# Performance work log

Measured on AMD Instinct MI355X. Metric: run time of the kernel, lower is better.

The kernel has to match this reference:

```python
import jax, jax.numpy as jnp
import numpy as np

B, D, M, C = 1024, 64, 3, 16384

def setup_inputs() -> dict:
    key = jax.random.key(0)
    ks = jax.random.split(key, 8)
    # unit-norm features (as in contrastive learning) keep exp() in range
    f = jax.random.normal(ks[0], (B, D), jnp.float32)
    f_I = jax.random.normal(ks[1], (B, D), jnp.float32)
    f = f / jnp.linalg.norm(f, axis=1, keepdims=True)
    f_I = f_I / jnp.linalg.norm(f_I, axis=1, keepdims=True)
    cen = jax.random.normal(ks[2], (M, C, D), jnp.float32)
    cen_I = jax.random.normal(ks[3], (M, C, D), jnp.float32)
    cen = cen / jnp.linalg.norm(cen, axis=2, keepdims=True)
    cen_I = cen_I / jnp.linalg.norm(cen_I, axis=2, keepdims=True)
    # concentrations in [0.5, 1.5): positive temperatures
    conc = jax.random.uniform(ks[4], (M, C), jnp.float32) + 0.5
    conc_I = jax.random.uniform(ks[5], (M, C), jnp.float32) + 0.5
    lab = jax.random.randint(ks[6], (M, B), 0, C, jnp.int64 if jax.config.jax_enable_x64 else jnp.int32)
    lab_I = jax.random.randint(ks[7], (M, B), 0, C, jnp.int64 if jax.config.jax_enable_x64 else jnp.int32)
    return {"features": f, "features_I": f_I, "M_kmeans": cen, "M_kmeans_I": cen_I,
            "concentrations": conc, "concentrations_I": conc_I,
            "labels": lab, "labels_I": lab_I, "lb": 1}

def _branch_loss(centroids, feats, conc, labels):
    # centroids: [M,C,D], feats: [B,D], conc: [M,C], labels: [M,B]
    # logits[m,c,b] = (centroids[m,c] . feats[b]) / conc[m,c]
    logits = jnp.einsum('mcd,bd->mcb', centroids, feats) / conc[:, :, None]
    exp_logits = jnp.exp(logits)                       # [M,C,B]
    log_sum = jnp.sum(exp_logits, axis=1)              # [M,B]
    pos = jnp.take_along_axis(exp_logits, labels[:, None, :], axis=1)[:, 0, :]  # [M,B]
    return jnp.sum(jnp.log(pos / log_sum))             # scalar (summed over m and b)

def reference(features, features_I, M_kmeans, M_kmeans_I,
              concentrations, concentrations_I, labels, labels_I, lb):
    m_num = M_kmeans.shape[0]
    batch_size = features.shape[0]
    t = _branch_loss(M_kmeans, features_I, concentrations, labels)
    t_I = _branch_loss(M_kmeans_I, features, concentrations_I, labels_I)
    return (1.0 / batch_size) * lb * (-1.0 / m_num) * 0.5 * (t + t_I)
```

## Files before the change

### kernel.cpp

```cpp
#include <hip/hip_runtime.h>

#define B_   1024
#define D_   64
#define M_   3
#define C_   16384
#define NCH  32
#define CCH  (C_ / NCH)
#define NTL  (CCH / 16)

typedef __attribute__((ext_vector_type(8))) short bf16x8;
typedef __attribute__((ext_vector_type(4))) float f32x4;

__device__ __forceinline__ unsigned bfpack2(float lo, float hi) {
    return __builtin_amdgcn_perm(__float_as_uint(hi), __float_as_uint(lo),
                                 0x07060302u);
}
__device__ __forceinline__ bf16x8 pack8(float4 x, float4 y) {
    union { unsigned u[4]; bf16x8 v; } r;
    r.u[0] = bfpack2(x.x, x.y);
    r.u[1] = bfpack2(x.z, x.w);
    r.u[2] = bfpack2(y.x, y.y);
    r.u[3] = bfpack2(y.z, y.w);
    return r.v;
}
__device__ __forceinline__ float fexp2(float x) {
    float r; asm("v_exp_f32 %0, %1" : "=v"(r) : "v"(x)); return r;
}
__device__ __forceinline__ void gll16(const void* g, void* l) {
    __builtin_amdgcn_global_load_lds(
        (const __attribute__((address_space(1))) void*)g,
        (__attribute__((address_space(3))) void*)l, 16, 0, 0);
}


__global__ __launch_bounds__(256) void prep(
    const float* __restrict__ f, const float* __restrict__ f_I,
    unsigned short* __restrict__ fbf)
{
    const int t    = blockIdx.x * 256 + threadIdx.x;
    const int br   = t >> 13;
    const int r    = t & 8191;
    const int bt   = r >> 7;
    const int h    = (r >> 6) & 1;
    const int lane = r & 63;
    const int b    = bt * 16 + (lane & 15);
    const int d0   = h * 32 + (lane >> 4) * 8;
    const float* src = (br ? f : f_I) + (size_t)b * D_ + d0;
    const float4 x = *reinterpret_cast<const float4*>(src);
    const float4 y = *reinterpret_cast<const float4*>(src + 4);
    *reinterpret_cast<bf16x8*>(fbf + (size_t)t * 8) = pack8(x, y);
}

__global__ __launch_bounds__(256, 3) void lse_mfma(
    const float* __restrict__ cen0, const float* __restrict__ cen1,
    const unsigned short* __restrict__ fbf,
    const float* __restrict__ conc0, const float* __restrict__ conc1,
    float* __restrict__ wsum)
{
    __shared__ float tbuf[2][1024];
    __shared__ float cbuf[CCH];
    __shared__ float lsum[4][64];

    const int bid    = blockIdx.x;
    const int xcd    = bid & 7;
    const int i2     = bid >> 3;
    const int pp     = i2 >> 2;
    const int bblk   = i2 & 3;
    const int combo  = xcd * 24 + pp;
    const int cchunk = combo & 31;
    const int mbr    = combo >> 5;
    const int br = mbr & 1, m = mbr >> 1;

    const float* __restrict__ cen  = br ? cen1  : cen0;
    const float* __restrict__ conc = br ? conc1 : conc0;

    const int tid  = threadIdx.x;
    const int wv   = tid >> 6;
    const int lane = tid & 63;
    const int lrow = lane & 15;
    const int lk   = lane >> 4;
    const int wbase = bblk * 256 + wv * 64;
    const float LOG2E = 1.44269504088896340736f;

    const unsigned short* fbb = fbf + (size_t)br * 8192 * 8;
    bf16x8 af[4][2];
#pragma unroll
    for (int t = 0; t < 4; ++t)
#pragma unroll
        for (int h = 0; h < 2; ++h)
            af[t][h] = *reinterpret_cast<const bf16x8*>(
                fbb + ((size_t)(((wbase >> 4) + t) * 2 + h) * 64 + lane) * 8);

    const int cb = cchunk * CCH;
    const int srow = tid >> 4;
    const int soff = ((tid & 15) << 4) ^ ((srow & 7) << 4);
    const char* csrc = (const char*)(cen + ((size_t)m * C_ + cb) * D_)
                     + srow * 256 + soff;

    gll16(csrc, (char*)tbuf[0] + wv * 1024);
    if (tid < 128)
        gll16((const char*)(conc + (size_t)m * C_ + cb) + tid * 16,
              (char*)cbuf + wv * 1024);
    __syncthreads();

    float s[4][4];
#pragma unroll
    for (int t = 0; t < 4; ++t)
#pragma unroll
        for (int j = 0; j < 4; ++j) s[t][j] = 0.0f;

    const unsigned swz = (unsigned)((lrow & 7) << 4);
    int cur = 0;
    for (int ct = 0; ct < NTL; ++ct) {
        if (ct + 1 < NTL)
            gll16(csrc + (size_t)(ct + 1) * 4096,
                  (char*)tbuf[cur ^ 1] + wv * 1024);

        const char* bp = (const char*)tbuf[cur] + lrow * 256;
        const float4 r00 = *(const float4*)(bp + ((lk * 32      ) ^ swz));
        const float4 r01 = *(const float4*)(bp + ((lk * 32 + 16 ) ^ swz));
        const float4 r10 = *(const float4*)(bp + ((128 + lk * 32     ) ^ swz));
        const float4 r11 = *(const float4*)(bp + ((128 + lk * 32 + 16) ^ swz));
        const float  cc  = cbuf[ct * 16 + lrow];

        const bf16x8 bk0 = pack8(r00, r01);
        const bf16x8 bk1 = pack8(r10, r11);
        const float  ic  = LOG2E * __builtin_amdgcn_rcpf(cc);

        f32x4 a0 = {0.f,0.f,0.f,0.f}, a1 = {0.f,0.f,0.f,0.f};
        f32x4 a2 = {0.f,0.f,0.f,0.f}, a3 = {0.f,0.f,0.f,0.f};
        a0 = __builtin_amdgcn_mfma_f32_16x16x32_bf16(af[0][0], bk0, a0, 0, 0, 0);
        a0 = __builtin_amdgcn_mfma_f32_16x16x32_bf16(af[0][1], bk1, a0, 0, 0, 0);
        a1 = __builtin_amdgcn_mfma_f32_16x16x32_bf16(af[1][0], bk0, a1, 0, 0, 0);
        a1 = __builtin_amdgcn_mfma_f32_16x16x32_bf16(af[1][1], bk1, a1, 0, 0, 0);
        a2 = __builtin_amdgcn_mfma_f32_16x16x32_bf16(af[2][0], bk0, a2, 0, 0, 0);
        a2 = __builtin_amdgcn_mfma_f32_16x16x32_bf16(af[2][1], bk1, a2, 0, 0, 0);
        a3 = __builtin_amdgcn_mfma_f32_16x16x32_bf16(af[3][0], bk0, a3, 0, 0, 0);
        a3 = __builtin_amdgcn_mfma_f32_16x16x32_bf16(af[3][1], bk1, a3, 0, 0, 0);

#pragma unroll
        for (int j = 0; j < 4; ++j) {
            s[0][j] += fexp2(a0[j] * ic);
            s[1][j] += fexp2(a1[j] * ic);
            s[2][j] += fexp2(a2[j] * ic);
            s[3][j] += fexp2(a3[j] * ic);
        }

        __syncthreads();
        cur ^= 1;
    }

#pragma unroll
    for (int t = 0; t < 4; ++t)
#pragma unroll
        for (int j = 0; j < 4; ++j) {
            float v = s[t][j];
            v += __shfl_xor(v, 1);
            v += __shfl_xor(v, 2);
            v += __shfl_xor(v, 4);
            v += __shfl_xor(v, 8);
            s[t][j] = v;
        }
    if (lrow == 0) {
#pragma unroll
        for (int t = 0; t < 4; ++t)
#pragma unroll
            for (int j = 0; j < 4; ++j)
                lsum[wv][t * 16 + lk * 4 + j] = s[t][j];
    }
    __syncthreads();
    atomicAdd(&wsum[(size_t)(br * M_ + m) * B_ + bblk * 256 + tid],
              lsum[tid >> 6][tid & 63]);
}

__global__ __launch_bounds__(256) void finish(
    const float* __restrict__ f,    const float* __restrict__ f_I,
    const float* __restrict__ cen0, const float* __restrict__ cen1,
    const float* __restrict__ conc0,const float* __restrict__ conc1,
    const int*   __restrict__ lab0, const int*   __restrict__ lab1,
    const float* __restrict__ wsum, const int* __restrict__ lb,
    float* __restrict__ out)
{
    const int idx = blockIdx.x * 256 + threadIdx.x;
    const int br  = idx / (M_ * B_);
    const int r   = idx - br * (M_ * B_);
    const int m   = r / B_;
    const int b   = r - m * B_;

    const float* cen  = br ? cen1  : cen0;
    const float* conc = br ? conc1 : conc0;
    const int*   lab  = br ? lab1  : lab0;
    const float* ft   = br ? f     : f_I;

    const int c = lab[r];
    const float* cr   = cen + (size_t)(m * C_ + c) * D_;
    const float* frow = ft + (size_t)b * D_;
    float a0 = 0.f, a1 = 0.f, a2 = 0.f, a3 = 0.f;
#pragma unroll
    for (int d = 0; d < D_; d += 4) {
        a0 = fmaf(cr[d + 0], frow[d + 0], a0);
        a1 = fmaf(cr[d + 1], frow[d + 1], a1);
        a2 = fmaf(cr[d + 2], frow[d + 2], a2);
        a3 = fmaf(cr[d + 3], frow[d + 3], a3);
    }
    const float logit = ((a0 + a1) + (a2 + a3)) / conc[(size_t)m * C_ + c];
    float term = logit - __logf(wsum[idx]);

#pragma unroll
    for (int off = 32; off > 0; off >>= 1)
        term += __shfl_down(term, off);
    if ((threadIdx.x & 63) == 0) {
        const float scale = -0.5f * (float)lb[0] / (float)(B_ * M_);
        atomicAdd(out, scale * term);
    }
}

extern "C" void kernel_launch(void* const* d_in, const int* in_sizes, int n_in,
                              void* d_out, int out_size, void* d_ws, size_t ws_size,
                              hipStream_t stream) {
    const float* f      = (const float*)d_in[0];
    const float* f_I    = (const float*)d_in[1];
    const float* cen    = (const float*)d_in[2];
    const float* cen_I  = (const float*)d_in[3];
    const float* conc   = (const float*)d_in[4];
    const float* conc_I = (const float*)d_in[5];
    const int*   lab    = (const int*)d_in[6];
    const int*   lab_I  = (const int*)d_in[7];
    const int*   lb     = (const int*)d_in[8];

    float* ws   = (float*)d_ws;
    float* wsum = ws;
    unsigned short* fbf = (unsigned short*)(ws + 6144);
    float* out  = (float*)d_out;

    hipMemsetAsync(wsum, 0, 6144 * sizeof(float), stream);
    hipMemsetAsync(out, 0, sizeof(float), stream);

    prep<<<64, 256, 0, stream>>>(f, f_I, fbf);

    lse_mfma<<<768, 256, 0, stream>>>(cen, cen_I, fbf, conc, conc_I, wsum);

    finish<<<(2 * M_ * B_) / 256, 256, 0, stream>>>(
        f, f_I, cen, cen_I, conc, conc_I, lab, lab_I, wsum, lb, out);
}
```

Measured before the change: 125.4 us.

## Stage 64-row centroid tiles per barrier and fold memsets into prep kernel

Each pipeline stage now loads 64 centroid rows (four 16-row subtiles) into a larger double-buffered LDS area, so there are four times fewer barriers per chunk. Concentrations are now read straight from global memory instead of being staged in LDS. The two hipMemsetAsync calls are removed and their zeroing moves into the prep kernel, which cuts launch overhead. The cost is higher LDS use per block (32KB of tile buffers), which may reduce occupancy.

New measurement: 118.3 us. -5.7%, faster.

```diff
diff --git a/kernel.cpp b/kernel.cpp
--- a/kernel.cpp
+++ b/kernel.cpp
@@ -6,7 +6,8 @@
 #define C_   16384
 #define NCH  32
 #define CCH  (C_ / NCH)
-#define NTL  (CCH / 16)
+#define TROWS 64
+#define NTL  (CCH / TROWS)
 
 typedef __attribute__((ext_vector_type(8))) short bf16x8;
 typedef __attribute__((ext_vector_type(4))) float f32x4;
@@ -35,7 +36,8 @@
 
 __global__ __launch_bounds__(256) void prep(
     const float* __restrict__ f, const float* __restrict__ f_I,
-    unsigned short* __restrict__ fbf)
+    unsigned short* __restrict__ fbf, float* __restrict__ wsum,
+    float* __restrict__ out)
 {
     const int t    = blockIdx.x * 256 + threadIdx.x;
     const int br   = t >> 13;
@@ -49,6 +51,8 @@
     const float4 x = *reinterpret_cast<const float4*>(src);
     const float4 y = *reinterpret_cast<const float4*>(src + 4);
     *reinterpret_cast<bf16x8*>(fbf + (size_t)t * 8) = pack8(x, y);
+    if (t < 2 * M_ * B_) wsum[t] = 0.0f;
+    if (t == 16383) out[0] = 0.0f;
 }
 
 __global__ __launch_bounds__(256, 3) void lse_mfma(
@@ -57,8 +61,7 @@
     const float* __restrict__ conc0, const float* __restrict__ conc1,
     float* __restrict__ wsum)
 {
-    __shared__ float tbuf[2][1024];
-    __shared__ float cbuf[CCH];
+    __shared__ float tbuf[2][4096];
     __shared__ float lsum[4][64];
 
     const int bid    = blockIdx.x;
@@ -92,15 +95,18 @@
                 fbb + ((size_t)(((wbase >> 4) + t) * 2 + h) * 64 + lane) * 8);
 
     const int cb = cchunk * CCH;
-    const int srow = tid >> 4;
-    const int soff = ((tid & 15) << 4) ^ ((srow & 7) << 4);
-    const char* csrc = (const char*)(cen + ((size_t)m * C_ + cb) * D_)
-                     + srow * 256 + soff;
-
-    gll16(csrc, (char*)tbuf[0] + wv * 1024);
-    if (tid < 128)
-        gll16((const char*)(conc + (size_t)m * C_ + cb) + tid * 16,
-              (char*)cbuf + wv * 1024);
+    const char* cbase = (const char*)(cen + ((size_t)m * C_ + cb) * D_);
+    int soff[4];
+#pragma unroll
+    for (int s2 = 0; s2 < 4; ++s2) {
+        const int row = s2 * 16 + (tid >> 4);
+        soff[s2] = row * 256 + ((((tid & 15) << 4)) ^ ((row & 7) << 4));
+    }
+    const int dseg = wv * 1024;
+
+#pragma unroll
+    for (int s2 = 0; s2 < 4; ++s2)
+        gll16(cbase + soff[s2], (char*)tbuf[0] + s2 * 4096 + dseg);
     __syncthreads();
 
     float s[4][4];
@@ -110,42 +116,47 @@
         for (int j = 0; j < 4; ++j) s[t][j] = 0.0f;
 
     const unsigned swz = (unsigned)((lrow & 7) << 4);
+    const float* ccp = conc + (size_t)m * C_ + cb + lrow;
     int cur = 0;
     for (int ct = 0; ct < NTL; ++ct) {
-        if (ct + 1 < NTL)
-            gll16(csrc + (size_t)(ct + 1) * 4096,
-                  (char*)tbuf[cur ^ 1] + wv * 1024);
-
-        const char* bp = (const char*)tbuf[cur] + lrow * 256;
-        const float4 r00 = *(const float4*)(bp + ((lk * 32      ) ^ swz));
-        const float4 r01 = *(const float4*)(bp + ((lk * 32 + 16 ) ^ swz));
-        const float4 r10 = *(const float4*)(bp + ((128 + lk * 32     ) ^ swz));
-        const float4 r11 = *(const float4*)(bp + ((128 + lk * 32 + 16) ^ swz));
-        const float  cc  = cbuf[ct * 16 + lrow];
-
-        const bf16x8 bk0 = pack8(r00, r01);
-        const bf16x8 bk1 = pack8(r10, r11);
-        const float  ic  = LOG2E * __builtin_amdgcn_rcpf(cc);
-
-        f32x4 a0 = {0.f,0.f,0.f,0.f}, a1 = {0.f,0.f,0.f,0.f};
-        f32x4 a2 = {0.f,0.f,0.f,0.f}, a3 = {0.f,0.f,0.f,0.f};
-        a0 = __builtin_amdgcn_mfma_f32_16x16x32_bf16(af[0][0], bk0, a0, 0, 0, 0);
-        a0 = __builtin_amdgcn_mfma_f32_16x16x32_bf16(af[0][1], bk1, a0, 0, 0, 0);
-        a1 = __builtin_amdgcn_mfma_f32_16x16x32_bf16(af[1][0], bk0, a1, 0, 0, 0);
-        a1 = __builtin_amdgcn_mfma_f32_16x16x32_bf16(af[1][1], bk1, a1, 0, 0, 0);
-        a2 = __builtin_amdgcn_mfma_f32_16x16x32_bf16(af[2][0], bk0, a2, 0, 0, 0);
-        a2 = __builtin_amdgcn_mfma_f32_16x16x32_bf16(af[2][1], bk1, a2, 0, 0, 0);
-        a3 = __builtin_amdgcn_mfma_f32_16x16x32_bf16(af[3][0], bk0, a3, 0, 0, 0);
-        a3 = __builtin_amdgcn_mfma_f32_16x16x32_bf16(af[3][1], bk1, a3, 0, 0, 0);
-
-#pragma unroll
-        for (int j = 0; j < 4; ++j) {
-            s[0][j] += fexp2(a0[j] * ic);
-            s[1][j] += fexp2(a1[j] * ic);
-            s[2][j] += fexp2(a2[j] * ic);
-            s[3][j] += fexp2(a3[j] * ic);
+        if (ct + 1 < NTL) {
+#pragma unroll
+            for (int s2 = 0; s2 < 4; ++s2)
+                gll16(cbase + (size_t)(ct + 1) * 16384 + soff[s2],
+                      (char*)tbuf[cur ^ 1] + s2 * 4096 + dseg);
         }
-
+#pragma unroll
+        for (int st = 0; st < 4; ++st) {
+            const char* bp = (const char*)tbuf[cur] + st * 4096 + lrow * 256;
+            const float4 r00 = *(const float4*)(bp + ((lk * 32      ) ^ swz));
+            const float4 r01 = *(const float4*)(bp + ((lk * 32 + 16 ) ^ swz));
+            const float4 r10 = *(const float4*)(bp + ((128 + lk * 32     ) ^ swz));
+            const float4 r11 = *(const float4*)(bp + ((128 + lk * 32 + 16) ^ swz));
+            const float  cc  = ccp[ct * 64 + st * 16];
+
+            const bf16x8 bk0 = pack8(r00, r01);
+            const bf16x8 bk1 = pack8(r10, r11);
+            const float  ic  = LOG2E * __builtin_amdgcn_rcpf(cc);
+
+            f32x4 a0 = {0.f,0.f,0.f,0.f}, a1 = {0.f,0.f,0.f,0.f};
+            f32x4 a2 = {0.f,0.f,0.f,0.f}, a3 = {0.f,0.f,0.f,0.f};
+            a0 = __builtin_amdgcn_mfma_f32_16x16x32_bf16(af[0][0], bk0, a0, 0, 0, 0);
+            a0 = __builtin_amdgcn_mfma_f32_16x16x32_bf16(af[0][1], bk1, a0, 0, 0, 0);
+            a1 = __builtin_amdgcn_mfma_f32_16x16x32_bf16(af[1][0], bk0, a1, 0, 0, 0);
+            a1 = __builtin_amdgcn_mfma_f32_16x16x32_bf16(af[1][1], bk1, a1, 0, 0, 0);
+            a2 = __builtin_amdgcn_mfma_f32_16x16x32_bf16(af[2][0], bk0, a2, 0, 0, 0);
+            a2 = __builtin_amdgcn_mfma_f32_16x16x32_bf16(af[2][1], bk1, a2, 0, 0, 0);
+            a3 = __builtin_amdgcn_mfma_f32_16x16x32_bf16(af[3][0], bk0, a3, 0, 0, 0);
+            a3 = __builtin_amdgcn_mfma_f32_16x16x32_bf16(af[3][1], bk1, a3, 0, 0, 0);
+
+#pragma unroll
+            for (int j = 0; j < 4; ++j) {
+                s[0][j] += fexp2(a0[j] * ic);
+                s[1][j] += fexp2(a1[j] * ic);
+                s[2][j] += fexp2(a2[j] * ic);
+                s[3][j] += fexp2(a3[j] * ic);
+            }
+        }
         __syncthreads();
         cur ^= 1;
     }
@@ -233,10 +244,7 @@
     unsigned short* fbf = (unsigned short*)(ws + 6144);
     float* out  = (float*)d_out;
 
-    hipMemsetAsync(wsum, 0, 6144 * sizeof(float), stream);
-    hipMemsetAsync(out, 0, sizeof(float), stream);
-
-    prep<<<64, 256, 0, stream>>>(f, f_I, fbf);
+    prep<<<64, 256, 0, stream>>>(f, f_I, fbf, wsum, out);
 
     lse_mfma<<<768, 256, 0, stream>>>(cen, cen_I, fbf, conc, conc_I, wsum);
 
```
